# Performance work log

Measured on AMD Instinct MI355X. Metric: run time of the kernel, lower is better.

Reference implementation:

```python
import jax, jax.numpy as jnp
import numpy as np

NEAR, FAR = 0.2, 6.0
N_SAMPLES, N_IMPORTANCE = 64, 64
SPEED_FACTOR = 10.0
VOXEL_SIZE = 0.04
N_VOX = (128, 128, 128)
NUM_CLS = 20


def setup_inputs() -> dict:
    key = jax.random.key(0)
    k1, k2, k3, k4 = jax.random.split(key, 4)
    B, R = 1, 4096
    o = jax.random.uniform(k1, (B, R, 3), jnp.float32, 1.0, 4.0)  # origins inside the 5.12m volume
    d = jax.random.normal(k2, (B, R, 3), jnp.float32)
    rays = jnp.concatenate([o, d], -1)
    volume_attr_pred = jax.random.normal(k3, (B, 3 + NUM_CLS) + N_VOX, jnp.float32)
    volume_sdf = jax.random.normal(k4, (B, 1) + N_VOX, jnp.float32) * 0.1
    ln_beta = jnp.array([np.log(0.1) / SPEED_FACTOR], jnp.float32)
    return {"rays": rays, "volume_attr_pred": volume_attr_pred,
            "volume_sdf": volume_sdf, "ln_beta": ln_beta}


def _trilinear(vol, coords, align_corners, zeros_pad):
    """vol: [C, Dx, Dy, Dz]; coords: [N, 3] normalized to [-1, 1] per axis.
    Matches torch.nn.functional.grid_sample semantics (zeros / border padding)."""
    idxs, i0, frac = [], [], []
    for a in range(3):
        s = vol.shape[1 + a]
        c = coords[:, a]
        ia = (c + 1.0) * 0.5 * (s - 1) if align_corners else ((c + 1.0) * s - 1.0) * 0.5
        if not zeros_pad:  # border padding == clamp the source coordinate
            ia = jnp.clip(ia, 0.0, float(s - 1))
        idxs.append(ia)
        f = jnp.floor(ia)
        i0.append(f)
        frac.append(ia - f)
    res = jnp.zeros((vol.shape[0], coords.shape[0]), coords.dtype)
    for corner in range(8):
        w = jnp.ones_like(idxs[0])
        valid = jnp.ones(idxs[0].shape, bool)
        gi = []
        for a in range(3):
            off = (corner >> a) & 1
            ia = i0[a] + off
            w = w * (frac[a] if off else (1.0 - frac[a]))
            s = vol.shape[1 + a]
            valid = valid & (ia >= 0) & (ia <= s - 1)
            gi.append(jnp.clip(ia, 0, s - 1).astype(jnp.int32))
        if zeros_pad:
            w = jnp.where(valid, w, 0.0)
        vals = vol[:, gi[0], gi[1], gi[2]]  # [C, N]
        res = res + vals * w[None]
    return res.T  # [N, C]


def query_attrs(vap, pts_norm):  # grid_sample, bilinear, zeros, align_corners=False
    return jax.vmap(lambda v, c: _trilinear(v, c, False, True))(vap, pts_norm)


def query_sdf(vs, pts_norm):  # grid_sample, bilinear, border, align_corners=True
    return jax.vmap(lambda v, c: _trilinear(v, c, True, False))(vs, pts_norm)[..., 0]


def sdf2weights(sdf, d, alpha, beta):
    """VolSDF-style: sigma = alpha * Psi_beta(-sdf), then alpha-compositing."""
    e = jnp.exp(-jnp.abs(sdf) / beta)
    sigma = alpha * jnp.where(sdf >= 0, 0.5 * e, 1.0 - 0.5 * e)
    deltas = jnp.concatenate([d[..., 1:] - d[..., :-1],
                              jnp.full_like(d[..., :1], 1e10)], -1)
    a = 1.0 - jnp.exp(-sigma * deltas)
    T = jnp.cumprod(jnp.concatenate([jnp.ones_like(a[..., :1]), 1.0 - a + 1e-10], -1)[..., :-1], -1)
    return a * T


def sample_pdf(bins, weights, n):
    """Deterministic inverse-CDF sampling. bins [..., M], weights [..., M-1]."""
    w = weights + 1e-5
    pdf = w / w.sum(-1, keepdims=True)
    cdf = jnp.concatenate([jnp.zeros_like(pdf[..., :1]), jnp.cumsum(pdf, -1)], -1)  # [..., M]
    u = (jnp.arange(n, dtype=bins.dtype) + 0.5) / n
    shp = cdf.shape[:-1]
    cdf2 = cdf.reshape(-1, cdf.shape[-1])
    u2 = jnp.broadcast_to(u, shp + (n,)).reshape(-1, n)
    inds = jax.vmap(lambda c, uu: jnp.searchsorted(c, uu, side='right'))(cdf2, u2)
    M = cdf.shape[-1]
    below = jnp.clip(inds - 1, 0, M - 1)
    above = jnp.clip(inds, 0, M - 1)
    bins2 = bins.reshape(-1, bins.shape[-1])
    cg0 = jnp.take_along_axis(cdf2, below, -1)
    cg1 = jnp.take_along_axis(cdf2, above, -1)
    bg0 = jnp.take_along_axis(bins2, below, -1)
    bg1 = jnp.take_along_axis(bins2, above, -1)
    denom = jnp.where(cg1 - cg0 < 1e-5, 1.0, cg1 - cg0)
    t = (u2 - cg0) / denom
    return (bg0 + t * (bg1 - bg0)).reshape(shp + (n,))


def _forward(rays, volume_attr_pred, volume_sdf, ln_beta):
    rays_o, rays_d = rays[..., :3], rays[..., 3:6]
    rays_d = jnp.where(jnp.abs(rays_d) < 1e-6, 1e-6, rays_d)
    depth_ratio = jnp.linalg.norm(rays_d, axis=-1)  # [B, R]
    rays_d = rays_d / depth_ratio[..., None]
    B, R = rays_o.shape[:2]
    beta = jnp.exp(ln_beta[0] * SPEED_FACTOR)
    alpha = 1.0 / beta
    nxyz = jnp.asarray(N_VOX, jnp.float32) * VOXEL_SIZE  # scene extent per axis

    def normalize(p):
        return 2.0 * (p / nxyz) - 1.0

    t = jnp.linspace(0.0, 1.0, N_SAMPLES, dtype=jnp.float32)
    d_coarse = jnp.broadcast_to(NEAR * (1 - t) + FAR * t, (B, R, N_SAMPLES))

    # hierarchical fine sampling (under torch.no_grad in the original)
    t4 = jnp.linspace(0.0, 1.0, N_SAMPLES * 4, dtype=jnp.float32)
    d_init = jnp.broadcast_to(NEAR * (1 - t4) + FAR * t4, (B, R, N_SAMPLES * 4))
    pts_i = rays_o[..., None, :] + rays_d[..., None, :] * d_init[..., None]
    sdf_i = query_sdf(volume_sdf, normalize(pts_i).reshape(B, -1, 3)).reshape(B, R, -1)
    w_i = sdf2weights(sdf_i, d_init, alpha, beta)
    d_fine = jax.lax.stop_gradient(sample_pdf(d_init, w_i[..., :-1], N_IMPORTANCE))

    d_all = jnp.sort(jnp.concatenate([d_coarse, d_fine], -1), -1)  # [B, R, P]
    P = d_all.shape[-1]
    pts = rays_o[..., None, :] + rays_d[..., None, :] * d_all[..., None]
    xn_flat = normalize(pts).reshape(B, -1, 3)
    attrs = query_attrs(volume_attr_pred, xn_flat).reshape(B, R, P, -1)
    sdf = query_sdf(volume_sdf, xn_flat).reshape(B, R, P)
    valid = sdf.sum(-1) != P
    tau = sdf2weights(sdf, d_all, alpha, beta)
    rgb = jnp.sum(tau[..., None] * attrs[..., :3], -2)
    sem = jnp.sum(tau[..., None] * attrs[..., 3:], -2)
    dist = jnp.sum(tau / (tau.sum(-1, keepdims=True) + 1e-10) * d_all, -1)
    depth = dist / depth_ratio
    return rgb, depth, valid, sem


def reference(rays, volume_attr_pred, volume_sdf, ln_beta):
    return _forward(rays, volume_attr_pred, volume_sdf, ln_beta)
```

## Files before the change

### kernel.cpp

```cpp
#include <hip/hip_runtime.h>
#include <hip/hip_fp16.h>
#include <math.h>

#define DIM 128
#define VOXSTRIDE (DIM*DIM*DIM)
#define CATT 23
#define NEARF 0.2f
#define FARF 6.0f
#define REC_BYTES 64ull
#define WS_NEED (VOXSTRIDE * REC_BYTES)

__device__ __forceinline__ float d_init_val(int i) {
    float t = (float)i * (1.0f / 255.0f);
    return NEARF * (1.0f - t) + FARF * t;
}
__device__ __forceinline__ float d_coarse_val(int i) {
    float t = (float)i * (1.0f / 63.0f);
    return NEARF * (1.0f - t) + FARF * t;
}

__device__ __forceinline__ void setup_ac_border(float x, float y, float z,
                                                float* i0, float* fr) {
    float c[3] = {x, y, z};
#pragma unroll
    for (int a = 0; a < 3; a++) {
        float v = (c[a] + 1.0f) * 0.5f * 127.0f;
        v = fminf(fmaxf(v, 0.0f), 127.0f);
        float f = floorf(v);
        i0[a] = f;
        fr[a] = v - f;
    }
}
__device__ __forceinline__ void setup_nac_zeros(float x, float y, float z,
                                                float* i0, float* fr) {
    float c[3] = {x, y, z};
#pragma unroll
    for (int a = 0; a < 3; a++) {
        float v = ((c[a] + 1.0f) * 128.0f - 1.0f) * 0.5f;
        float f = floorf(v);
        i0[a] = f;
        fr[a] = v - f;
    }
}

__device__ __forceinline__ float tri_sdf_vol(const float* __restrict__ vol,
                                             float x, float y, float z) {
    float i0[3], fr[3];
    setup_ac_border(x, y, z, i0, fr);
    float res = 0.0f;
#pragma unroll
    for (int corner = 0; corner < 8; corner++) {
        float w = 1.0f;
        int gi[3];
#pragma unroll
        for (int a = 0; a < 3; a++) {
            int off = (corner >> a) & 1;
            float iv = i0[a] + (float)off;
            w *= off ? fr[a] : (1.0f - fr[a]);
            iv = fminf(fmaxf(iv, 0.0f), 127.0f);
            gi[a] = (int)iv;
        }
        int idx = (gi[0] * DIM + gi[1]) * DIM + gi[2];
        res += vol[idx] * w;
    }
    return res;
}

__device__ __forceinline__ float tri_sdf_rec(const float* __restrict__ recf,
                                             float x, float y, float z) {
    float i0[3], fr[3];
    setup_ac_border(x, y, z, i0, fr);
    float res = 0.0f;
#pragma unroll
    for (int corner = 0; corner < 8; corner++) {
        float w = 1.0f;
        int gi[3];
#pragma unroll
        for (int a = 0; a < 3; a++) {
            int off = (corner >> a) & 1;
            float iv = i0[a] + (float)off;
            w *= off ? fr[a] : (1.0f - fr[a]);
            iv = fminf(fmaxf(iv, 0.0f), 127.0f);
            gi[a] = (int)iv;
        }
        int idx = (gi[0] * DIM + gi[1]) * DIM + gi[2];
        res += recf[idx * 16 + 12] * w;
    }
    return res;
}

__device__ __forceinline__ void unpack16(uint4 a, uint4 b, float* v) {
    unsigned us[8] = {a.x, a.y, a.z, a.w, b.x, b.y, b.z, b.w};
#pragma unroll
    for (int i = 0; i < 8; i++) {
        v[2 * i]     = __half2float(__ushort_as_half((unsigned short)(us[i] & 0xffffu)));
        v[2 * i + 1] = __half2float(__ushort_as_half((unsigned short)(us[i] >> 16)));
    }
}

__device__ __forceinline__ void tri_attr_rec(const uint4* __restrict__ recs,
                                             float x, float y, float z,
                                             float* acc, int half) {
    float i0[3], fr[3];
    setup_nac_zeros(x, y, z, i0, fr);
#pragma unroll
    for (int corner = 0; corner < 8; corner++) {
        float w = 1.0f;
        bool valid = true;
        int gi[3];
#pragma unroll
        for (int a = 0; a < 3; a++) {
            int off = (corner >> a) & 1;
            float iv = i0[a] + (float)off;
            w *= off ? fr[a] : (1.0f - fr[a]);
            valid = valid && (iv >= 0.0f) && (iv <= 127.0f);
            iv = fminf(fmaxf(iv, 0.0f), 127.0f);
            gi[a] = (int)iv;
        }
        if (!valid) continue;
        int idx = (gi[0] * DIM + gi[1]) * DIM + gi[2];
        const uint4* q = recs + (size_t)idx * 4 + half;
        uint4 qa = q[0], qb = q[1];
        float vals[16];
        unpack16(qa, qb, vals);
        if (half == 0) {
#pragma unroll
            for (int c = 0; c < 12; c++) acc[c] += w * vals[c];
        } else {
#pragma unroll
            for (int c = 0; c < 11; c++) acc[c] += w * vals[c + 4];
        }
    }
}

__device__ __forceinline__ void tri_attr_planes(const float* __restrict__ vol,
                                                float x, float y, float z,
                                                float* acc, int half) {
    float i0[3], fr[3];
    setup_nac_zeros(x, y, z, i0, fr);
    int c0 = half ? 12 : 0;
    int nc = half ? 11 : 12;
#pragma unroll
    for (int corner = 0; corner < 8; corner++) {
        float w = 1.0f;
        bool valid = true;
        int gi[3];
#pragma unroll
        for (int a = 0; a < 3; a++) {
            int off = (corner >> a) & 1;
            float iv = i0[a] + (float)off;
            w *= off ? fr[a] : (1.0f - fr[a]);
            valid = valid && (iv >= 0.0f) && (iv <= 127.0f);
            iv = fminf(fmaxf(iv, 0.0f), 127.0f);
            gi[a] = (int)iv;
        }
        if (!valid) continue;
        int idx = (gi[0] * DIM + gi[1]) * DIM + gi[2];
        for (int c = 0; c < nc; c++)
            acc[c] += w * vol[(c0 + c) * VOXSTRIDE + idx];
    }
}

__global__ __launch_bounds__(256) void repack_kernel(
    const float* __restrict__ attr, const float* __restrict__ sdfv,
    uint4* __restrict__ recs) {
    int v = blockIdx.x * 256 + threadIdx.x;
    unsigned u[12];
#pragma unroll
    for (int p = 0; p < 12; p++) {
        float a = (2 * p < CATT) ? attr[(2 * p) * VOXSTRIDE + v] : 0.0f;
        float b = (2 * p + 1 < CATT) ? attr[(2 * p + 1) * VOXSTRIDE + v] : 0.0f;
        unsigned lo = (unsigned)__half_as_ushort(__float2half(a));
        unsigned hi = (unsigned)__half_as_ushort(__float2half(b));
        u[p] = lo | (hi << 16);
    }
    float s = sdfv[v];
    uint4* dst = recs + (size_t)v * 4;
    dst[0] = make_uint4(u[0], u[1], u[2], u[3]);
    dst[1] = make_uint4(u[4], u[5], u[6], u[7]);
    dst[2] = make_uint4(u[8], u[9], u[10], u[11]);
    dst[3] = make_uint4(__float_as_uint(s), 0u, 0u, 0u);
}

__device__ __forceinline__ int incl_scan_prod(float (*buf)[256], int n, int tid) {
    int cur = 0;
    for (int off = 1; off < n; off <<= 1) {
        int nxt = cur ^ 1;
        if (tid < n) {
            float v = buf[cur][tid];
            if (tid >= off) v *= buf[cur][tid - off];
            buf[nxt][tid] = v;
        }
        __syncthreads();
        cur = nxt;
    }
    return cur;
}
__device__ __forceinline__ int incl_scan_add(float (*buf)[256], int n, int tid) {
    int cur = 0;
    for (int off = 1; off < n; off <<= 1) {
        int nxt = cur ^ 1;
        if (tid < n) {
            float v = buf[cur][tid];
            if (tid >= off) v += buf[cur][tid - off];
            buf[nxt][tid] = v;
        }
        __syncthreads();
        cur = nxt;
    }
    return cur;
}

template <bool PACKED>
__global__ __launch_bounds__(256) void volrender_kernel(
    const float* __restrict__ rays,
    const float* __restrict__ attr,
    const float* __restrict__ sdfv,
    const uint4* __restrict__ recs,
    const float* __restrict__ lnb,
    float* __restrict__ out, int R) {
    __shared__ float s_scan[2][256];
    __shared__ float s_cdf[256];
    __shared__ float s_dfine[64];
    __shared__ float s_dall[128];
    __shared__ float s_red[26][129];
    __shared__ float s_sum[26];
    __shared__ float s_xn[3][128];
    __shared__ float s_tau[128];

    const int r = blockIdx.x;
    const int tid = threadIdx.x;

    float ox = rays[r * 6 + 0], oy = rays[r * 6 + 1], oz = rays[r * 6 + 2];
    float dx = rays[r * 6 + 3], dy = rays[r * 6 + 4], dz = rays[r * 6 + 5];
    dx = (fabsf(dx) < 1e-6f) ? 1e-6f : dx;
    dy = (fabsf(dy) < 1e-6f) ? 1e-6f : dy;
    dz = (fabsf(dz) < 1e-6f) ? 1e-6f : dz;
    float dr = sqrtf(dx * dx + dy * dy + dz * dz);
    float invdr = 1.0f / dr;
    dx *= invdr; dy *= invdr; dz *= invdr;

    const float beta = expf(lnb[0] * 10.0f);
    const float alpha = 1.0f / beta;
    const float innorm = 2.0f / 5.12f;

    float d0 = d_init_val(tid);
    float sdf0;
    {
        float px = ox + dx * d0, py = oy + dy * d0, pz = oz + dz * d0;
        sdf0 = tri_sdf_vol(sdfv, px * innorm - 1.0f, py * innorm - 1.0f,
                           pz * innorm - 1.0f);
    }
    float delta0 = (tid < 255) ? (d_init_val(tid + 1) - d0) : 1e10f;
    float e0 = expf(-fabsf(sdf0) / beta);
    float sig0 = alpha * ((sdf0 >= 0.0f) ? 0.5f * e0 : (1.0f - 0.5f * e0));
    float tr0 = expf(-sig0 * delta0);
    float a0 = 1.0f - tr0;
    s_scan[0][tid] = tr0 + 1e-10f;
    __syncthreads();
    int cur = incl_scan_prod(s_scan, 256, tid);
    float T0 = (tid == 0) ? 1.0f : s_scan[cur][tid - 1];
    float w0 = a0 * T0;
    __syncthreads();
    s_scan[0][tid] = (tid < 255) ? (w0 + 1e-5f) : 0.0f;
    __syncthreads();
    cur = incl_scan_add(s_scan, 256, tid);
    float wsum = s_scan[cur][254];
    float invw = 1.0f / wsum;
    if (tid == 0) s_cdf[0] = 0.0f;
    else s_cdf[tid] = s_scan[cur][tid - 1] * invw;
    __syncthreads();

    if (tid < 64) {
        float u = ((float)tid + 0.5f) * (1.0f / 64.0f);
        int lo = 0, hi = 256;
        while (lo < hi) {
            int m = (lo + hi) >> 1;
            if (s_cdf[m] <= u) lo = m + 1; else hi = m;
        }
        int below = lo - 1; if (below > 255) below = 255; if (below < 0) below = 0;
        int above = lo;     if (above > 255) above = 255;
        float cg0 = s_cdf[below], cg1 = s_cdf[above];
        float bg0 = d_init_val(below), bg1 = d_init_val(above);
        float den = cg1 - cg0;
        if (den < 1e-5f) den = 1.0f;
        float t = (u - cg0) / den;
        s_dfine[tid] = bg0 + t * (bg1 - bg0);
    }
    __syncthreads();

    if (tid < 64) {
        float v = d_coarse_val(tid);
        int lo = 0, hi = 64;
        while (lo < hi) {
            int m = (lo + hi) >> 1;
            if (s_dfine[m] < v) lo = m + 1; else hi = m;
        }
        s_dall[tid + lo] = v;
    } else if (tid < 128) {
        int j = tid - 64;
        float v = s_dfine[j];
        int lo = 0, hi = 64;
        while (lo < hi) {
            int m = (lo + hi) >> 1;
            if (d_coarse_val(m) <= v) lo = m + 1; else hi = m;
        }
        s_dall[j + lo] = v;
    }
    __syncthreads();

    float dall = 0.0f;
    if (tid < 128) {
        dall = s_dall[tid];
        float px = ox + dx * dall, py = oy + dy * dall, pz = oz + dz * dall;
        float xnx = px * innorm - 1.0f;
        float xny = py * innorm - 1.0f;
        float xnz = pz * innorm - 1.0f;
        s_xn[0][tid] = xnx; s_xn[1][tid] = xny; s_xn[2][tid] = xnz;
        float sdf2 = PACKED ? tri_sdf_rec((const float*)recs, xnx, xny, xnz)
                            : tri_sdf_vol(sdfv, xnx, xny, xnz);
        s_red[25][tid] = sdf2;
        float delta2 = (tid < 127) ? (s_dall[tid + 1] - dall) : 1e10f;
        float e2 = expf(-fabsf(sdf2) / beta);
        float sig2 = alpha * ((sdf2 >= 0.0f) ? 0.5f * e2 : (1.0f - 0.5f * e2));
        float tr2 = expf(-sig2 * delta2);
        s_scan[0][tid] = tr2 + 1e-10f;
        s_red[23][tid] = 1.0f - tr2;
    }
    __syncthreads();
    cur = incl_scan_prod(s_scan, 128, tid);
    if (tid < 128) {
        float T2 = (tid == 0) ? 1.0f : s_scan[cur][tid - 1];
        float tau = s_red[23][tid] * T2;
        s_tau[tid] = tau;
    }
    __syncthreads();

    {
        int samp = tid & 127;
        int half = tid >> 7;
        float tau = s_tau[samp];
        float xnx = s_xn[0][samp], xny = s_xn[1][samp], xnz = s_xn[2][samp];
        float acc[12];
#pragma unroll
        for (int c = 0; c < 12; c++) acc[c] = 0.0f;
        if (tau != 0.0f) {
            if (PACKED) tri_attr_rec(recs, xnx, xny, xnz, acc, half);
            else        tri_attr_planes(attr, xnx, xny, xnz, acc, half);
        }
        int c0 = half ? 12 : 0;
        int nc = half ? 11 : 12;
        for (int c = 0; c < nc; c++) s_red[c0 + c][samp] = tau * acc[c];
        if (half == 0) {
            s_red[23][samp] = tau;
            s_red[24][samp] = tau * dall;
        }
    }
    __syncthreads();

    if (tid < 26) {
        float s = 0.0f;
        for (int p = 0; p < 128; p++) s += s_red[tid][p];
        s_sum[tid] = s;
    }
    __syncthreads();

    if (tid < 3) {
        out[r * 3 + tid] = s_sum[tid];
    } else if (tid < 23) {
        out[5 * R + r * 20 + (tid - 3)] = s_sum[tid];
    } else if (tid == 23) {
        float dist = s_sum[24] / (s_sum[23] + 1e-10f);
        out[3 * R + r] = dist / dr;
    } else if (tid == 24) {
        out[4 * R + r] = (s_sum[25] != 128.0f) ? 1.0f : 0.0f;
    }
}

extern "C" void kernel_launch(void* const* d_in, const int* in_sizes, int n_in,
                              void* d_out, int out_size, void* d_ws, size_t ws_size,
                              hipStream_t stream) {
    const float* rays = (const float*)d_in[0];
    const float* attr = (const float*)d_in[1];
    const float* sdfv = (const float*)d_in[2];
    const float* lnb  = (const float*)d_in[3];
    float* out = (float*)d_out;
    int R = in_sizes[0] / 6;

    bool packed = (ws_size >= WS_NEED) && (((uintptr_t)d_ws & 15) == 0);
    if (packed) {
        uint4* recs = (uint4*)d_ws;
        repack_kernel<<<dim3(VOXSTRIDE / 256), dim3(256), 0, stream>>>(attr, sdfv, recs);
        volrender_kernel<true><<<dim3(R), dim3(256), 0, stream>>>(
            rays, attr, sdfv, recs, lnb, out, R);
    } else {
        volrender_kernel<false><<<dim3(R), dim3(256), 0, stream>>>(
            rays, attr, sdfv, (const uint4*)nullptr, lnb, out, R);
    }
}
```

Before: 424.7 us.

## Replace shared-memory scans and reductions with wavefront shuffles; overlap attr gathers

Replaces the barrier-heavy shared-memory Hillis-Steele scans and the serial 128-element column reductions with 64-lane shuffle scans and reductions plus small cross-wave fixups. Attribute gathers are issued before the transmittance scan, so they overlap with the SDF computation, but they are no longer skipped when tau is zero. The repack kernel now loads all channels first with nontemporal loads and stores, and packs pairs to half2. The launch bound adds a minimum-occupancy hint, which may constrain register allocation.

```diff
diff --git a/kernel.cpp b/kernel.cpp
--- a/kernel.cpp
+++ b/kernel.cpp
@@ -7,8 +7,9 @@
 #define CATT 23
 #define NEARF 0.2f
 #define FARF 6.0f
-#define REC_BYTES 64ull
-#define WS_NEED (VOXSTRIDE * REC_BYTES)
+#define WS_NEED ((size_t)VOXSTRIDE * 64ull)
+
+typedef unsigned uintv4 __attribute__((ext_vector_type(4)));
 
 __device__ __forceinline__ float d_init_val(int i) {
     float t = (float)i * (1.0f / 255.0f);
@@ -27,8 +28,7 @@
         float v = (c[a] + 1.0f) * 0.5f * 127.0f;
         v = fminf(fmaxf(v, 0.0f), 127.0f);
         float f = floorf(v);
-        i0[a] = f;
-        fr[a] = v - f;
+        i0[a] = f; fr[a] = v - f;
     }
 }
 __device__ __forceinline__ void setup_nac_zeros(float x, float y, float z,
@@ -38,8 +38,7 @@
     for (int a = 0; a < 3; a++) {
         float v = ((c[a] + 1.0f) * 128.0f - 1.0f) * 0.5f;
         float f = floorf(v);
-        i0[a] = f;
-        fr[a] = v - f;
+        i0[a] = f; fr[a] = v - f;
     }
 }
 
@@ -89,7 +88,7 @@
     return res;
 }
 
-__device__ __forceinline__ void unpack16(uint4 a, uint4 b, float* v) {
+__device__ __forceinline__ void unpack16(uintv4 a, uintv4 b, float* v) {
     unsigned us[8] = {a.x, a.y, a.z, a.w, b.x, b.y, b.z, b.w};
 #pragma unroll
     for (int i = 0; i < 8; i++) {
@@ -98,7 +97,7 @@
     }
 }
 
-__device__ __forceinline__ void tri_attr_rec(const uint4* __restrict__ recs,
+__device__ __forceinline__ void tri_attr_rec(const uintv4* __restrict__ recs,
                                              float x, float y, float z,
                                              float* acc, int half) {
     float i0[3], fr[3];
@@ -119,8 +118,8 @@
         }
         if (!valid) continue;
         int idx = (gi[0] * DIM + gi[1]) * DIM + gi[2];
-        const uint4* q = recs + (size_t)idx * 4 + half;
-        uint4 qa = q[0], qb = q[1];
+        const uintv4* q = recs + (size_t)idx * 4 + half;
+        uintv4 qa = q[0], qb = q[1];
         float vals[16];
         unpack16(qa, qb, vals);
         if (half == 0) {
@@ -163,73 +162,75 @@
 
 __global__ __launch_bounds__(256) void repack_kernel(
     const float* __restrict__ attr, const float* __restrict__ sdfv,
-    uint4* __restrict__ recs) {
+    uintv4* __restrict__ recs) {
     int v = blockIdx.x * 256 + threadIdx.x;
+    float a[24];
+#pragma unroll
+    for (int c = 0; c < CATT; c++)
+        a[c] = __builtin_nontemporal_load(attr + (size_t)c * VOXSTRIDE + v);
+    a[23] = 0.0f;
+    float s = sdfv[v];
     unsigned u[12];
 #pragma unroll
     for (int p = 0; p < 12; p++) {
-        float a = (2 * p < CATT) ? attr[(2 * p) * VOXSTRIDE + v] : 0.0f;
-        float b = (2 * p + 1 < CATT) ? attr[(2 * p + 1) * VOXSTRIDE + v] : 0.0f;
-        unsigned lo = (unsigned)__half_as_ushort(__float2half(a));
-        unsigned hi = (unsigned)__half_as_ushort(__float2half(b));
-        u[p] = lo | (hi << 16);
-    }
-    float s = sdfv[v];
-    uint4* dst = recs + (size_t)v * 4;
-    dst[0] = make_uint4(u[0], u[1], u[2], u[3]);
-    dst[1] = make_uint4(u[4], u[5], u[6], u[7]);
-    dst[2] = make_uint4(u[8], u[9], u[10], u[11]);
-    dst[3] = make_uint4(__float_as_uint(s), 0u, 0u, 0u);
-}
-
-__device__ __forceinline__ int incl_scan_prod(float (*buf)[256], int n, int tid) {
-    int cur = 0;
-    for (int off = 1; off < n; off <<= 1) {
-        int nxt = cur ^ 1;
-        if (tid < n) {
-            float v = buf[cur][tid];
-            if (tid >= off) v *= buf[cur][tid - off];
-            buf[nxt][tid] = v;
-        }
-        __syncthreads();
-        cur = nxt;
-    }
-    return cur;
-}
-__device__ __forceinline__ int incl_scan_add(float (*buf)[256], int n, int tid) {
-    int cur = 0;
-    for (int off = 1; off < n; off <<= 1) {
-        int nxt = cur ^ 1;
-        if (tid < n) {
-            float v = buf[cur][tid];
-            if (tid >= off) v += buf[cur][tid - off];
-            buf[nxt][tid] = v;
-        }
-        __syncthreads();
-        cur = nxt;
-    }
-    return cur;
+        __half2 h = __float22half2_rn(make_float2(a[2 * p], a[2 * p + 1]));
+        u[p] = __builtin_bit_cast(unsigned, h);
+    }
+    uintv4* dst = recs + (size_t)v * 4;
+    uintv4 q0 = {u[0], u[1], u[2], u[3]};
+    uintv4 q1 = {u[4], u[5], u[6], u[7]};
+    uintv4 q2 = {u[8], u[9], u[10], u[11]};
+    uintv4 q3 = {__float_as_uint(s), 0u, 0u, 0u};
+    __builtin_nontemporal_store(q0, dst);
+    __builtin_nontemporal_store(q1, dst + 1);
+    __builtin_nontemporal_store(q2, dst + 2);
+    __builtin_nontemporal_store(q3, dst + 3);
+}
+
+__device__ __forceinline__ float wave_scan_prod(float v, int lane) {
+#pragma unroll
+    for (int off = 1; off < 64; off <<= 1) {
+        float o = __shfl_up(v, off, 64);
+        if (lane >= off) v *= o;
+    }
+    return v;
+}
+__device__ __forceinline__ float wave_scan_add(float v, int lane) {
+#pragma unroll
+    for (int off = 1; off < 64; off <<= 1) {
+        float o = __shfl_up(v, off, 64);
+        if (lane >= off) v += o;
+    }
+    return v;
+}
+__device__ __forceinline__ float wave_reduce_add(float v) {
+#pragma unroll
+    for (int m = 32; m >= 1; m >>= 1) v += __shfl_xor(v, m, 64);
+    return v;
 }
 
 template <bool PACKED>
-__global__ __launch_bounds__(256) void volrender_kernel(
+__global__ __launch_bounds__(256, 4) void volrender_kernel(
     const float* __restrict__ rays,
     const float* __restrict__ attr,
     const float* __restrict__ sdfv,
-    const uint4* __restrict__ recs,
+    const uintv4* __restrict__ recs,
     const float* __restrict__ lnb,
     float* __restrict__ out, int R) {
-    __shared__ float s_scan[2][256];
     __shared__ float s_cdf[256];
     __shared__ float s_dfine[64];
     __shared__ float s_dall[128];
-    __shared__ float s_red[26][129];
-    __shared__ float s_sum[26];
     __shared__ float s_xn[3][128];
     __shared__ float s_tau[128];
+    __shared__ float s_pA[4], s_pB[4];
+    __shared__ float s_pC;
+    __shared__ float s_wred[4][16];
+    __shared__ float s_sum[26];
 
     const int r = blockIdx.x;
     const int tid = threadIdx.x;
+    const int lane = tid & 63;
+    const int wv = tid >> 6;
 
     float ox = rays[r * 6 + 0], oy = rays[r * 6 + 1], oz = rays[r * 6 + 2];
     float dx = rays[r * 6 + 3], dy = rays[r * 6 + 4], dz = rays[r * 6 + 5];
@@ -256,19 +257,33 @@
     float sig0 = alpha * ((sdf0 >= 0.0f) ? 0.5f * e0 : (1.0f - 0.5f * e0));
     float tr0 = expf(-sig0 * delta0);
     float a0 = 1.0f - tr0;
-    s_scan[0][tid] = tr0 + 1e-10f;
-    __syncthreads();
-    int cur = incl_scan_prod(s_scan, 256, tid);
-    float T0 = (tid == 0) ? 1.0f : s_scan[cur][tid - 1];
+
+    float inclp = wave_scan_prod(tr0 + 1e-10f, lane);
+    if (lane == 63) s_pA[wv] = inclp;
+    __syncthreads();
+    float offp = 1.0f;
+#pragma unroll
+    for (int j = 0; j < 3; j++) if (j < wv) offp *= s_pA[j];
+    float exclp = __shfl_up(inclp, 1, 64);
+    if (lane == 0) exclp = 1.0f;
+    float T0 = exclp * offp;
     float w0 = a0 * T0;
-    __syncthreads();
-    s_scan[0][tid] = (tid < 255) ? (w0 + 1e-5f) : 0.0f;
-    __syncthreads();
-    cur = incl_scan_add(s_scan, 256, tid);
-    float wsum = s_scan[cur][254];
-    float invw = 1.0f / wsum;
-    if (tid == 0) s_cdf[0] = 0.0f;
-    else s_cdf[tid] = s_scan[cur][tid - 1] * invw;
+
+    float wp = (tid < 255) ? (w0 + 1e-5f) : 0.0f;
+    float incla = wave_scan_add(wp, lane);
+    if (lane == 63) s_pB[wv] = incla;
+    __syncthreads();
+    float offa = 0.0f, tot = 0.0f;
+#pragma unroll
+    for (int j = 0; j < 4; j++) {
+        float pj = s_pB[j];
+        tot += pj;
+        if (j < wv) offa += pj;
+    }
+    float excla = __shfl_up(incla, 1, 64);
+    if (lane == 0) excla = 0.0f;
+    float invw = 1.0f / tot;
+    s_cdf[tid] = (excla + offa) * invw;
     __syncthreads();
 
     if (tid < 64) {
@@ -309,58 +324,78 @@
     }
     __syncthreads();
 
-    float dall = 0.0f;
+    float dall = 0.0f, delta2 = 1e10f;
     if (tid < 128) {
         dall = s_dall[tid];
+        if (tid < 127) delta2 = s_dall[tid + 1] - dall;
         float px = ox + dx * dall, py = oy + dy * dall, pz = oz + dz * dall;
-        float xnx = px * innorm - 1.0f;
-        float xny = py * innorm - 1.0f;
-        float xnz = pz * innorm - 1.0f;
-        s_xn[0][tid] = xnx; s_xn[1][tid] = xny; s_xn[2][tid] = xnz;
-        float sdf2 = PACKED ? tri_sdf_rec((const float*)recs, xnx, xny, xnz)
-                            : tri_sdf_vol(sdfv, xnx, xny, xnz);
-        s_red[25][tid] = sdf2;
-        float delta2 = (tid < 127) ? (s_dall[tid + 1] - dall) : 1e10f;
+        s_xn[0][tid] = px * innorm - 1.0f;
+        s_xn[1][tid] = py * innorm - 1.0f;
+        s_xn[2][tid] = pz * innorm - 1.0f;
+    }
+    __syncthreads();
+
+    const int samp = tid & 127;
+    const int half = tid >> 7;
+    float xnx = s_xn[0][samp], xny = s_xn[1][samp], xnz = s_xn[2][samp];
+
+    float sdf2 = 0.0f;
+    if (tid < 128)
+        sdf2 = PACKED ? tri_sdf_rec((const float*)recs, xnx, xny, xnz)
+                      : tri_sdf_vol(sdfv, xnx, xny, xnz);
+
+    float acc[12];
+#pragma unroll
+    for (int c = 0; c < 12; c++) acc[c] = 0.0f;
+    if (PACKED) tri_attr_rec(recs, xnx, xny, xnz, acc, half);
+    else        tri_attr_planes(attr, xnx, xny, xnz, acc, half);
+
+    float fv = 1.0f, a2 = 0.0f;
+    if (tid < 128) {
         float e2 = expf(-fabsf(sdf2) / beta);
         float sig2 = alpha * ((sdf2 >= 0.0f) ? 0.5f * e2 : (1.0f - 0.5f * e2));
         float tr2 = expf(-sig2 * delta2);
-        s_scan[0][tid] = tr2 + 1e-10f;
-        s_red[23][tid] = 1.0f - tr2;
-    }
-    __syncthreads();
-    cur = incl_scan_prod(s_scan, 128, tid);
+        a2 = 1.0f - tr2;
+        fv = tr2 + 1e-10f;
+    }
+    float incl3 = wave_scan_prod(fv, lane);
+    if (tid == 63) s_pC = incl3;
+    __syncthreads();
     if (tid < 128) {
-        float T2 = (tid == 0) ? 1.0f : s_scan[cur][tid - 1];
-        float tau = s_red[23][tid] * T2;
+        float offp2 = (wv == 0) ? 1.0f : s_pC;
+        float ex = __shfl_up(incl3, 1, 64);
+        if (lane == 0) ex = 1.0f;
+        float tau = a2 * ex * offp2;
         s_tau[tid] = tau;
     }
     __syncthreads();
-
-    {
-        int samp = tid & 127;
-        int half = tid >> 7;
-        float tau = s_tau[samp];
-        float xnx = s_xn[0][samp], xny = s_xn[1][samp], xnz = s_xn[2][samp];
-        float acc[12];
-#pragma unroll
-        for (int c = 0; c < 12; c++) acc[c] = 0.0f;
-        if (tau != 0.0f) {
-            if (PACKED) tri_attr_rec(recs, xnx, xny, xnz, acc, half);
-            else        tri_attr_planes(attr, xnx, xny, xnz, acc, half);
-        }
-        int c0 = half ? 12 : 0;
-        int nc = half ? 11 : 12;
-        for (int c = 0; c < nc; c++) s_red[c0 + c][samp] = tau * acc[c];
-        if (half == 0) {
-            s_red[23][samp] = tau;
-            s_red[24][samp] = tau * dall;
-        }
+    float tau = s_tau[samp];
+
+    float red[15];
+#pragma unroll
+    for (int c = 0; c < 15; c++) red[c] = 0.0f;
+    if (half == 0) {
+#pragma unroll
+        for (int c = 0; c < 12; c++) red[c] = tau * acc[c];
+        red[12] = tau;
+        red[13] = tau * dall;
+        red[14] = sdf2;
+    } else {
+#pragma unroll
+        for (int c = 0; c < 11; c++) red[c] = tau * acc[c];
+    }
+#pragma unroll
+    for (int c = 0; c < 15; c++) {
+        float v = wave_reduce_add(red[c]);
+        if (lane == 0) s_wred[wv][c] = v;
     }
     __syncthreads();
 
     if (tid < 26) {
-        float s = 0.0f;
-        for (int p = 0; p < 128; p++) s += s_red[tid][p];
+        float s;
+        if (tid < 12)      s = s_wred[0][tid] + s_wred[1][tid];
+        else if (tid < 23) s = s_wred[2][tid - 12] + s_wred[3][tid - 12];
+        else               s = s_wred[0][tid - 11] + s_wred[1][tid - 11];
         s_sum[tid] = s;
     }
     __syncthreads();
@@ -389,12 +424,12 @@
 
     bool packed = (ws_size >= WS_NEED) && (((uintptr_t)d_ws & 15) == 0);
     if (packed) {
-        uint4* recs = (uint4*)d_ws;
+        uintv4* recs = (uintv4*)d_ws;
         repack_kernel<<<dim3(VOXSTRIDE / 256), dim3(256), 0, stream>>>(attr, sdfv, recs);
         volrender_kernel<true><<<dim3(R), dim3(256), 0, stream>>>(
             rays, attr, sdfv, recs, lnb, out, R);
     } else {
         volrender_kernel<false><<<dim3(R), dim3(256), 0, stream>>>(
-            rays, attr, sdfv, (const uint4*)nullptr, lnb, out, R);
-    }
-}
+            rays, attr, sdfv, (const uintv4*)nullptr, lnb, out, R);
+    }
+}
```

Result: slower. 497.3 us (+17.1%).
